# Kernel optimization log

Measured on AMD Instinct MI355X. Metric: run time of the kernel, lower is better.

Reference implementation:

```python
import jax, jax.numpy as jnp
import numpy as np
from jax import lax

RADIUS = 0.3
NSAMPLE = 16
NPOINT = 1024
NH = 1   # num_heading_bin
NS = 18  # num_size_cluster
EPS = 1e-5  # torch BatchNorm eps


def _bn(x, g, b, m, v):
    # eval-mode batchnorm over the last (channel) axis
    return (x - m) * (g / jnp.sqrt(v + EPS)) + b


def _fps(xyz, npoint):
    # furthest point sampling; xyz: (B,K,3) -> (B,npoint) int32 indices
    B, K, _ = xyz.shape
    def body(carry, _):
        dists, far = carry
        cur = jnp.take_along_axis(xyz, far[:, None, None], axis=1)  # (B,1,3)
        d = jnp.sum((xyz - cur) ** 2, -1)                           # (B,K)
        dists = jnp.minimum(dists, d)
        nxt = jnp.argmax(dists, -1).astype(jnp.int32)
        return (dists, nxt), far
    init = (jnp.full((B, K), 1e10, xyz.dtype), jnp.zeros((B,), jnp.int32))
    _, inds = lax.scan(body, init, None, length=npoint)
    return jnp.swapaxes(inds, 0, 1)  # (B, npoint)


def _ball_query(xyz, new_xyz):
    # first-NSAMPLE points within RADIUS of each center, pad with first hit
    K = xyz.shape[1]
    d2 = jnp.sum((new_xyz[:, :, None, :] - xyz[:, None, :, :]) ** 2, -1)  # (B,S,K)
    mask = d2 < RADIUS ** 2
    idx = jnp.where(mask, jnp.arange(K, dtype=jnp.int32)[None, None, :], K)
    idx = jnp.sort(idx, -1)[..., :NSAMPLE]
    first = idx[..., :1]
    idx = jnp.where(idx == K, first, idx)
    idx = jnp.where(idx == K, 0, idx)  # degenerate: no neighbor at all
    return idx  # (B,S,NSAMPLE)


def setup_inputs() -> dict:
    key = jax.random.key(0)
    ks = jax.random.split(key, 32)
    inp = {}
    inp['xyz'] = jax.random.normal(ks[0], (8, 8192, 3), jnp.float32)
    inp['features'] = jax.random.normal(ks[1], (8, 256, 8192), jnp.float32)
    i = 2
    # shared MLP: 259 -> 128 -> 128 -> 128 (conv2d 1x1, no bias, then BN)
    for l, (o, c) in enumerate([(128, 259), (128, 128), (128, 128)]):
        inp[f'mlp_w{l}'] = jax.random.normal(ks[i], (o, c), jnp.float32) * 0.1; i += 1
        inp[f'mlp_g{l}'] = jnp.ones((o,), jnp.float32)
        inp[f'mlp_b{l}'] = jnp.zeros((o,), jnp.float32)
        inp[f'mlp_m{l}'] = jax.random.normal(ks[i], (o,), jnp.float32) * 0.01; i += 1
        inp[f'mlp_v{l}'] = jax.random.uniform(ks[i], (o,), jnp.float32, 0.5, 1.5); i += 1
    # box head convs (conv1d k=1)
    for nm, (o, c) in [('c1', (128, 128)), ('c2', (128, 128)), ('c3', (97, 128))]:
        inp[f'{nm}_w'] = jax.random.normal(ks[i], (o, c), jnp.float32) * 0.1; i += 1
        inp[f'{nm}_b'] = jnp.zeros((o,), jnp.float32)
    for nm in ['bn1', 'bn2']:
        inp[f'{nm}_g'] = jnp.ones((128,), jnp.float32)
        inp[f'{nm}_b'] = jnp.zeros((128,), jnp.float32)
        inp[f'{nm}_m'] = jax.random.normal(ks[i], (128,), jnp.float32) * 0.01; i += 1
        inp[f'{nm}_v'] = jax.random.uniform(ks[i], (128,), jnp.float32, 0.5, 1.5); i += 1
    inp['mean_size_arr'] = jax.random.uniform(ks[i], (NS, 3), jnp.float32, 0.3, 2.0)
    return inp


def reference(xyz, features,
              mlp_w0, mlp_g0, mlp_b0, mlp_m0, mlp_v0,
              mlp_w1, mlp_g1, mlp_b1, mlp_m1, mlp_v1,
              mlp_w2, mlp_g2, mlp_b2, mlp_m2, mlp_v2,
              c1_w, c1_b, bn1_g, bn1_b, bn1_m, bn1_v,
              c2_w, c2_b, bn2_g, bn2_b, bn2_m, bn2_v,
              c3_w, c3_b, mean_size_arr):
    B = xyz.shape[0]
    # --- vote aggregation: FPS + ball query + group + shared MLP + maxpool ---
    fps_inds = _fps(xyz, NPOINT)
    new_xyz = jnp.take_along_axis(xyz, fps_inds[..., None], axis=1)  # (B,S,3)
    idx = _ball_query(xyz, new_xyz)                                  # (B,S,n)
    gather = jax.vmap(lambda a, i: a[i])
    g_xyz = (gather(xyz, idx) - new_xyz[:, :, None, :]) / RADIUS     # normalize_xyz
    g_f = gather(jnp.swapaxes(features, 1, 2), idx)                  # (B,S,n,256)
    h = jnp.concatenate([g_xyz, g_f], -1)                            # (B,S,n,259)
    for w, g, b, m, v in ((mlp_w0, mlp_g0, mlp_b0, mlp_m0, mlp_v0),
                          (mlp_w1, mlp_g1, mlp_b1, mlp_m1, mlp_v1),
                          (mlp_w2, mlp_g2, mlp_b2, mlp_m2, mlp_v2)):
        h = jax.nn.relu(_bn(jnp.einsum('bsnc,oc->bsno', h, w), g, b, m, v))
    feat = jnp.max(h, axis=2)                                        # (B,S,128)
    # --- box head (conv1d k=1 == per-point linear) ---
    net = jax.nn.relu(_bn(jnp.einsum('bsc,oc->bso', feat, c1_w) + c1_b,
                          bn1_g, bn1_b, bn1_m, bn1_v))
    net = jax.nn.relu(_bn(jnp.einsum('bsc,oc->bso', net, c2_w) + c2_b,
                          bn2_g, bn2_b, bn2_m, bn2_v))
    net = jnp.einsum('bsc,oc->bso', net, c3_w) + c3_b                # (B,S,97)
    # --- decode_scores ---
    obj = net[..., 0:2]
    center = new_xyz + net[..., 2:5]
    hs = net[..., 5:5 + NH]
    hr = net[..., 5 + NH:5 + 2 * NH] * (np.pi / NH)
    ss = net[..., 5 + 2 * NH:5 + 2 * NH + NS]
    srn = net[..., 5 + 2 * NH + NS:5 + 2 * NH + 4 * NS].reshape(B, NPOINT, NS, 3)
    sr = (srn * mean_size_arr[None, None]).reshape(B, NPOINT, NS * 3)
    sem = net[..., 5 + 2 * NH + 4 * NS:]
    return jnp.concatenate([obj, center, hs, hr, ss, sr, sem], -1)   # (B,S,97)
```

## Files before the change

### kernel.cpp

```cpp
#include <hip/hip_runtime.h>
#include <cstdint>
#include <cstddef>

#define BATCH   8
#define KPTS    8192
#define NPT     1024
#define NSAMP   16
#define RAD2    0.09f
#define HB      136
#define NWORK   248

typedef float f32x2 __attribute__((ext_vector_type(2)));
typedef float f32x4 __attribute__((ext_vector_type(4)));
typedef short s16x4 __attribute__((ext_vector_type(4)));
typedef short s16x8 __attribute__((ext_vector_type(8)));

__device__ __forceinline__ unsigned short f2bf(float x) {
    unsigned u = __float_as_uint(x);
    return (unsigned short)((u + 0x7fffu + ((u >> 16) & 1u)) >> 16);
}

template <int CTRL>
__device__ __forceinline__ float dppmaxf(float v) {
    int o = __builtin_amdgcn_update_dpp(0, __float_as_int(v), CTRL, 0xf, 0xf, true);
    return fmaxf(v, __int_as_float(o));
}

__device__ __forceinline__ int aload(int* p) {
    return __hip_atomic_load(p, __ATOMIC_ACQUIRE, __HIP_MEMORY_SCOPE_AGENT);
}
__device__ __forceinline__ void abump(int* p, int v) {
    __hip_atomic_fetch_add(p, v, __ATOMIC_RELEASE, __HIP_MEMORY_SCOPE_AGENT);
}

union __align__(16) SM {
    struct {
        float xs[KPTS], ys[KPTS], zs[KPTS];
        unsigned long long slot3[3];
        int hist[NPT];
    } fps;
    struct {
        float As[16 * 64];
        float Bs[16 * 130];
    } gemm;
    struct {
        unsigned short W1[128 * HB];
        unsigned short W2[128 * HB];
        unsigned short hbf[64 * HB];
        float gx[64], gy[64], gz[64];
        int   pidx[64];
        float s0[128], t0[128], wxs[128], wys[128], wzs[128];
        float s1[128], t1[128], s2[128], t2[128];
    } mlp;
};

__global__ __launch_bounds__(256, 1) void mega_kernel(
    const float* __restrict__ xyz, float* __restrict__ new_xyz,
    const float* __restrict__ feats, const float* __restrict__ w0,
    float* __restrict__ f0out,
    const float* __restrict__ g0, const float* __restrict__ b0,
    const float* __restrict__ m0, const float* __restrict__ v0,
    const float* __restrict__ w1,
    const float* __restrict__ g1, const float* __restrict__ b1a,
    const float* __restrict__ m1, const float* __restrict__ v1,
    const float* __restrict__ w2,
    const float* __restrict__ g2, const float* __restrict__ b2a,
    const float* __restrict__ m2, const float* __restrict__ v2,
    float* __restrict__ featout, int* __restrict__ cnt) {
    __shared__ SM sm;
    const int tid = threadIdx.x;
    const int bid = blockIdx.x;

    if (bid < 8) {
#pragma clang fp contract(off)
        const int b = bid;
        const float* xb = xyz + (size_t)b * KPTS * 3;

        for (int i = tid; i < KPTS; i += 256) {
            sm.fps.xs[i] = xb[i * 3 + 0];
            sm.fps.ys[i] = xb[i * 3 + 1];
            sm.fps.zs[i] = xb[i * 3 + 2];
        }
        if (tid < 3) sm.fps.slot3[tid] = 0ull;
        __syncthreads();

        const int base = tid << 5;
        f32x2 px[16], py[16], pz[16], dmn[16];
#pragma unroll
        for (int j = 0; j < 16; ++j) {
            int i0 = base + (j << 1);
            px[j] = (f32x2){sm.fps.xs[i0], sm.fps.xs[i0 + 1]};
            py[j] = (f32x2){sm.fps.ys[i0], sm.fps.ys[i0 + 1]};
            pz[j] = (f32x2){sm.fps.zs[i0], sm.fps.zs[i0 + 1]};
            dmn[j] = (f32x2){1e10f, 1e10f};
        }

        const int lane = tid & 63;
        int far = 0;
        int cur = 0, nxt = 1;
        for (int it = 0; it < NPT; ++it) {
            if (tid == 0) { sm.fps.hist[it] = far; sm.fps.slot3[nxt] = 0ull; }
            const float cx = sm.fps.xs[far], cy = sm.fps.ys[far], cz = sm.fps.zs[far];
            const f32x2 cx2 = (f32x2){cx, cx};
            const f32x2 cy2 = (f32x2){cy, cy};
            const f32x2 cz2 = (f32x2){cz, cz};

            f32x2 mm = (f32x2){-1.0f, -1.0f};
#pragma unroll
            for (int j = 0; j < 16; ++j) {
                f32x2 dx = px[j] - cx2;
                f32x2 dy = py[j] - cy2;
                f32x2 dz = pz[j] - cz2;
                f32x2 d  = (dx * dx + dy * dy) + dz * dz;
                f32x2 nd = __builtin_elementwise_min(dmn[j], d);
                dmn[j] = nd;
                mm = __builtin_elementwise_max(mm, nd);
            }
            float lmax = fmaxf(mm.x, mm.y);

            int ci = 0x7fffffff;
#pragma unroll
            for (int j = 0; j < 16; ++j) {
                if (dmn[j].x == lmax) ci = min(ci, base + (j << 1));
                if (dmn[j].y == lmax) ci = min(ci, base + (j << 1) + 1);
            }

            float wm = lmax;
            wm = dppmaxf<0x111>(wm);
            wm = dppmaxf<0x112>(wm);
            wm = dppmaxf<0x114>(wm);
            wm = dppmaxf<0x118>(wm);
            wm = dppmaxf<0x142>(wm);
            wm = dppmaxf<0x143>(wm);
            float wmax = __int_as_float(
                __builtin_amdgcn_readlane(__float_as_int(wm), 63));

            unsigned long long mk = __ballot(lmax == wmax);
            int wl = (int)__builtin_ctzll(mk);
            int cw = __builtin_amdgcn_readlane(ci, wl);

            if (lane == 0) {
                unsigned long long pk =
                    ((unsigned long long)__float_as_uint(wmax) << 32)
                    | (unsigned)(8191 - cw);
                atomicMax(&sm.fps.slot3[cur], pk);
            }
            __syncthreads();

            unsigned long long g = sm.fps.slot3[cur];
            far = 8191 - (int)(unsigned)(g & 0xffffffffull);
            cur = nxt;
            nxt = (nxt == 2) ? 0 : nxt + 1;

            if ((it & 31) == 31) {
                if (tid < 128) {
                    int c = tid & 3;
                    if (c < 3) {
                        int i = (it - 31) + (tid >> 2);
                        int idx = sm.fps.hist[i];
                        float v = (c == 0) ? sm.fps.xs[idx]
                                 : (c == 1) ? sm.fps.ys[idx] : sm.fps.zs[idx];
                        new_xyz[((size_t)b * NPT + i) * 3 + c] = v;
                    }
                }
                __threadfence();
                __syncthreads();
                if (tid == 0) abump(&cnt[b], 32);
            }
        }
        return;
    }

    const int wk = bid - 8;

    {
        const int rb = (tid >> 4) << 2;
        const int ob = tid & 15;
        for (int t = wk; t < 1024; t += NWORK) {
            const int b  = t >> 7;
            const int p0 = (t & 127) << 6;
            const float* fb = feats + (size_t)b * 256 * KPTS;

            float acc[4][8];
#pragma unroll
            for (int r = 0; r < 4; ++r)
#pragma unroll
                for (int c = 0; c < 8; ++c) acc[r][c] = 0.f;

            for (int k0 = 0; k0 < 256; k0 += 16) {
#pragma unroll
                for (int i = 0; i < 4; ++i) {
                    int e = tid + (i << 8);
                    int kk = e >> 6, pc = e & 63;
                    sm.gemm.As[kk * 64 + pc] = fb[(size_t)(k0 + kk) * KPTS + p0 + pc];
                }
#pragma unroll
                for (int i = 0; i < 8; ++i) {
                    int e = tid + (i << 8);
                    int o = e >> 4, kk = e & 15;
                    sm.gemm.Bs[kk * 130 + o] = w0[o * 259 + 3 + k0 + kk];
                }
                __syncthreads();
#pragma unroll
                for (int kk = 0; kk < 16; ++kk) {
                    float a[4], wvv[8];
#pragma unroll
                    for (int r = 0; r < 4; ++r) a[r] = sm.gemm.As[kk * 64 + rb + r];
#pragma unroll
                    for (int c = 0; c < 8; ++c) wvv[c] = sm.gemm.Bs[kk * 130 + ob + (c << 4)];
#pragma unroll
                    for (int r = 0; r < 4; ++r)
#pragma unroll
                        for (int c = 0; c < 8; ++c) acc[r][c] = fmaf(a[r], wvv[c], acc[r][c]);
                }
                __syncthreads();
            }
#pragma unroll
            for (int r = 0; r < 4; ++r) {
                float* outp = f0out + ((size_t)b * KPTS + p0 + rb + r) * 128 + ob;
#pragma unroll
                for (int c = 0; c < 8; ++c) outp[c << 4] = acc[r][c];
            }
        }
        __threadfence();
        __syncthreads();
        if (tid == 0) abump(&cnt[8], 1);
    }

    if (tid < 128) {
        float sc = g0[tid] / sqrtf(v0[tid] + 1e-5f);
        sm.mlp.s0[tid] = sc; sm.mlp.t0[tid] = b0[tid] - m0[tid] * sc;
        sc = g1[tid] / sqrtf(v1[tid] + 1e-5f);
        sm.mlp.s1[tid] = sc; sm.mlp.t1[tid] = b1a[tid] - m1[tid] * sc;
        sc = g2[tid] / sqrtf(v2[tid] + 1e-5f);
        sm.mlp.s2[tid] = sc; sm.mlp.t2[tid] = b2a[tid] - m2[tid] * sc;
        sm.mlp.wxs[tid] = w0[tid * 259 + 0];
        sm.mlp.wys[tid] = w0[tid * 259 + 1];
        sm.mlp.wzs[tid] = w0[tid * 259 + 2];
    }
#pragma unroll 4
    for (int i = 0; i < 16; ++i) {
        int e = tid + (i << 8);
        int o = e >> 5;
        int kt = (e & 31) << 2;
        float4 a4 = *(const float4*)(w1 + o * 128 + kt);
        s16x4 c4 = { (short)f2bf(a4.x), (short)f2bf(a4.y),
                     (short)f2bf(a4.z), (short)f2bf(a4.w) };
        *(s16x4*)&sm.mlp.W1[o * HB + kt] = c4;
        float4 b4 = *(const float4*)(w2 + o * 128 + kt);
        s16x4 d4 = { (short)f2bf(b4.x), (short)f2bf(b4.y),
                     (short)f2bf(b4.z), (short)f2bf(b4.w) };
        *(s16x4*)&sm.mlp.W2[o * HB + kt] = d4;
    }
    __syncthreads();

    const int lane = tid & 63;
    const int w    = tid >> 6;
    const int l15  = lane & 15;
    const int quad = lane >> 4;
    const int wrow = w << 4;

    for (int g = wk; g < 2048; g += NWORK) {
        const int b  = g & 7;
        const int qg = g >> 3;
        const int q0 = (b << 10) + (qg << 2);

        if (tid == 0) {
            while (aload(&cnt[8]) < NWORK) __builtin_amdgcn_s_sleep(16);
            const int need = (qg << 2) + 4;
            while (aload(&cnt[b]) < need) __builtin_amdgcn_s_sleep(16);
        }
        __syncthreads();

        {
            const int q = q0 + w;
            const float* xb = xyz + (size_t)b * KPTS * 3;
            const float qx = new_xyz[q * 3 + 0];
            const float qy = new_xyz[q * 3 + 1];
            const float qz = new_xyz[q * 3 + 2];
            int* op = &sm.mlp.pidx[w << 4];

            int total = 0;
            int first_p = 0;
            for (int c = 0; c < KPTS / 64; ++c) {
                int p = (c << 6) + lane;
                float pxv = xb[p * 3 + 0], pyv = xb[p * 3 + 1], pzv = xb[p * 3 + 2];
                float dx = __fsub_rn(qx, pxv), dy = __fsub_rn(qy, pyv), dz = __fsub_rn(qz, pzv);
                float d2 = __fadd_rn(__fadd_rn(__fmul_rn(dx, dx), __fmul_rn(dy, dy)),
                                     __fmul_rn(dz, dz));
                bool pred = d2 < RAD2;
                unsigned long long mask = __ballot(pred);
                if (total == 0 && mask != 0ull) first_p = (c << 6) + (int)__builtin_ctzll(mask);
                if (pred) {
                    int rank = (int)__popcll(mask & ((1ull << lane) - 1ull));
                    int slot = total + rank;
                    if (slot < NSAMP) op[slot] = p;
                }
                total += (int)__popcll(mask);
                if (total >= NSAMP) break;
            }
            if (total < NSAMP && lane >= total && lane < NSAMP) op[lane] = first_p;
        }
        __syncthreads();

        if (tid < 64) {
            int p = sm.mlp.pidx[tid];
            int q = q0 + (tid >> 4);
            const float* pp = xyz + ((size_t)b * KPTS + p) * 3;
            const float* nq = new_xyz + (size_t)q * 3;
            sm.mlp.gx[tid] = (pp[0] - nq[0]) / 0.3f;
            sm.mlp.gy[tid] = (pp[1] - nq[1]) / 0.3f;
            sm.mlp.gz[tid] = (pp[2] - nq[2]) / 0.3f;
        }
        __syncthreads();

#pragma unroll 2
        for (int i = 0; i < 8; ++i) {
            int e = tid + (i << 8);
            int row = e >> 5, o = (e & 31) << 2;
            int p = sm.mlp.pidx[row];
            float4 v4 = *(const float4*)(f0out + ((size_t)b * KPTS + p) * 128 + o);
            float gxr = sm.mlp.gx[row], gyr = sm.mlp.gy[row], gzr = sm.mlp.gz[row];
            float r0 = fmaf(sm.mlp.wzs[o + 0], gzr, fmaf(sm.mlp.wys[o + 0], gyr, fmaf(sm.mlp.wxs[o + 0], gxr, v4.x)));
            float r1 = fmaf(sm.mlp.wzs[o + 1], gzr, fmaf(sm.mlp.wys[o + 1], gyr, fmaf(sm.mlp.wxs[o + 1], gxr, v4.y)));
            float r2 = fmaf(sm.mlp.wzs[o + 2], gzr, fmaf(sm.mlp.wys[o + 2], gyr, fmaf(sm.mlp.wxs[o + 2], gxr, v4.z)));
            float r3 = fmaf(sm.mlp.wzs[o + 3], gzr, fmaf(sm.mlp.wys[o + 3], gyr, fmaf(sm.mlp.wxs[o + 3], gxr, v4.w)));
            s16x4 c4;
            c4.x = (short)f2bf(fmaxf(fmaf(r0, sm.mlp.s0[o + 0], sm.mlp.t0[o + 0]), 0.f));
            c4.y = (short)f2bf(fmaxf(fmaf(r1, sm.mlp.s0[o + 1], sm.mlp.t0[o + 1]), 0.f));
            c4.z = (short)f2bf(fmaxf(fmaf(r2, sm.mlp.s0[o + 2], sm.mlp.t0[o + 2]), 0.f));
            c4.w = (short)f2bf(fmaxf(fmaf(r3, sm.mlp.s0[o + 3], sm.mlp.t0[o + 3]), 0.f));
            *(s16x4*)&sm.mlp.hbf[row * HB + o] = c4;
        }
        __syncthreads();

        f32x4 acc[8];
#pragma unroll
        for (int t = 0; t < 8; ++t) acc[t] = (f32x4){0.f, 0.f, 0.f, 0.f};
#pragma unroll
        for (int k0 = 0; k0 < 128; k0 += 32) {
            s16x8 a = *(const s16x8*)&sm.mlp.hbf[(wrow + l15) * HB + k0 + (quad << 3)];
#pragma unroll
            for (int t = 0; t < 8; ++t) {
                s16x8 bf = *(const s16x8*)&sm.mlp.W1[((t << 4) + l15) * HB + k0 + (quad << 3)];
                acc[t] = __builtin_amdgcn_mfma_f32_16x16x32_bf16(a, bf, acc[t], 0, 0, 0);
            }
        }
        __syncthreads();

#pragma unroll
        for (int t = 0; t < 8; ++t) {
            int o = (t << 4) + l15;
            float ss = sm.mlp.s1[o], tt = sm.mlp.t1[o];
#pragma unroll
            for (int r = 0; r < 4; ++r) {
                float v = fmaxf(fmaf(acc[t][r], ss, tt), 0.f);
                sm.mlp.hbf[(wrow + (quad << 2) + r) * HB + o] = f2bf(v);
            }
        }
        __syncthreads();

#pragma unroll
        for (int t = 0; t < 8; ++t) acc[t] = (f32x4){0.f, 0.f, 0.f, 0.f};
#pragma unroll
        for (int k0 = 0; k0 < 128; k0 += 32) {
            s16x8 a = *(const s16x8*)&sm.mlp.hbf[(wrow + l15) * HB + k0 + (quad << 3)];
#pragma unroll
            for (int t = 0; t < 8; ++t) {
                s16x8 bf = *(const s16x8*)&sm.mlp.W2[((t << 4) + l15) * HB + k0 + (quad << 3)];
                acc[t] = __builtin_amdgcn_mfma_f32_16x16x32_bf16(a, bf, acc[t], 0, 0, 0);
            }
        }

#pragma unroll
        for (int t = 0; t < 8; ++t) {
            int o = (t << 4) + l15;
            float ss = sm.mlp.s2[o], tt = sm.mlp.t2[o];
            float m0v = fmaxf(fmaf(acc[t][0], ss, tt), 0.f);
            float m1v = fmaxf(fmaf(acc[t][1], ss, tt), 0.f);
            float m2v = fmaxf(fmaf(acc[t][2], ss, tt), 0.f);
            float m3v = fmaxf(fmaf(acc[t][3], ss, tt), 0.f);
            float m = fmaxf(fmaxf(m0v, m1v), fmaxf(m2v, m3v));
            m = fmaxf(m, __shfl_xor(m, 16));
            m = fmaxf(m, __shfl_xor(m, 32));
            if (quad == 0)
                featout[(size_t)(q0 + w) * 128 + o] = m;
        }
    }
}

__global__ __launch_bounds__(256) void head_kernel(
    const float* __restrict__ feat, const float* __restrict__ new_xyz,
    const float* __restrict__ c1w, const float* __restrict__ c1b,
    const float* __restrict__ c2w, const float* __restrict__ c2b,
    const float* __restrict__ c3w, const float* __restrict__ c3b,
    const float* __restrict__ bg1, const float* __restrict__ bb1,
    const float* __restrict__ bm1, const float* __restrict__ bv1,
    const float* __restrict__ bg2, const float* __restrict__ bb2,
    const float* __restrict__ bm2, const float* __restrict__ bv2,
    const float* __restrict__ msz, float* __restrict__ out) {
    const int tid = threadIdx.x;
    const int q0  = blockIdx.x << 3;
    __shared__ float fs[8][128], n1[8][128], n2[8][128];
    __shared__ float s1[128], t1[128], s2[128], t2[128], ms[54];

#pragma unroll
    for (int i = 0; i < 4; ++i) {
        int e = tid + (i << 8);
        fs[e >> 7][e & 127] = feat[(size_t)q0 * 128 + e];
    }
    if (tid < 128) {
        float sc = bg1[tid] / sqrtf(bv1[tid] + 1e-5f);
        s1[tid] = sc; t1[tid] = bb1[tid] - bm1[tid] * sc;
        sc = bg2[tid] / sqrtf(bv2[tid] + 1e-5f);
        s2[tid] = sc; t2[tid] = bb2[tid] - bm2[tid] * sc;
    }
    if (tid < 54) ms[tid] = msz[tid];
    __syncthreads();

    const int o    = tid & 127;
    const int half = tid >> 7;

    {
        float a[4];
#pragma unroll
        for (int j = 0; j < 4; ++j) a[j] = c1b[o];
        const float* wr = c1w + o * 128;
        for (int k = 0; k < 128; k += 4) {
            float4 w4 = *(const float4*)(wr + k);
#pragma unroll
            for (int j = 0; j < 4; ++j) {
                int qq = half * 4 + j;
                a[j] = fmaf(fs[qq][k + 0], w4.x, a[j]);
                a[j] = fmaf(fs[qq][k + 1], w4.y, a[j]);
                a[j] = fmaf(fs[qq][k + 2], w4.z, a[j]);
                a[j] = fmaf(fs[qq][k + 3], w4.w, a[j]);
            }
        }
#pragma unroll
        for (int j = 0; j < 4; ++j)
            n1[half * 4 + j][o] = fmaxf(fmaf(a[j], s1[o], t1[o]), 0.f);
    }
    __syncthreads();
    {
        float a[4];
#pragma unroll
        for (int j = 0; j < 4; ++j) a[j] = c2b[o];
        const float* wr = c2w + o * 128;
        for (int k = 0; k < 128; k += 4) {
            float4 w4 = *(const float4*)(wr + k);
#pragma unroll
            for (int j = 0; j < 4; ++j) {
                int qq = half * 4 + j;
                a[j] = fmaf(n1[qq][k + 0], w4.x, a[j]);
                a[j] = fmaf(n1[qq][k + 1], w4.y, a[j]);
                a[j] = fmaf(n1[qq][k + 2], w4.z, a[j]);
                a[j] = fmaf(n1[qq][k + 3], w4.w, a[j]);
            }
        }
#pragma unroll
        for (int j = 0; j < 4; ++j)
            n2[half * 4 + j][o] = fmaxf(fmaf(a[j], s2[o], t2[o]), 0.f);
    }
    __syncthreads();
    if (o < 97) {
        float a[4];
#pragma unroll
        for (int j = 0; j < 4; ++j) a[j] = c3b[o];
        const float* wr = c3w + o * 128;
        for (int k = 0; k < 128; k += 4) {
            float4 w4 = *(const float4*)(wr + k);
#pragma unroll
            for (int j = 0; j < 4; ++j) {
                int qq = half * 4 + j;
                a[j] = fmaf(n2[qq][k + 0], w4.x, a[j]);
                a[j] = fmaf(n2[qq][k + 1], w4.y, a[j]);
                a[j] = fmaf(n2[qq][k + 2], w4.z, a[j]);
                a[j] = fmaf(n2[qq][k + 3], w4.w, a[j]);
            }
        }
#pragma unroll
        for (int j = 0; j < 4; ++j) {
            int q = q0 + half * 4 + j;
            float v = a[j];
            if (o >= 2 && o < 5) v += new_xyz[(size_t)q * 3 + (o - 2)];
            else if (o == 6) v *= 3.14159265358979323846f;
            else if (o >= 25 && o < 79) v *= ms[o - 25];
            out[(size_t)q * 97 + o] = v;
        }
    }
}

extern "C" void kernel_launch(void* const* d_in, const int* in_sizes, int n_in,
                              void* d_out, int out_size, void* d_ws, size_t ws_size,
                              hipStream_t stream) {
    const float* xyz      = (const float*)d_in[0];
    const float* features = (const float*)d_in[1];
    const float* w0  = (const float*)d_in[2];
    const float* g0  = (const float*)d_in[3];
    const float* b0  = (const float*)d_in[4];
    const float* m0  = (const float*)d_in[5];
    const float* v0  = (const float*)d_in[6];
    const float* w1  = (const float*)d_in[7];
    const float* g1  = (const float*)d_in[8];
    const float* b1  = (const float*)d_in[9];
    const float* m1  = (const float*)d_in[10];
    const float* v1  = (const float*)d_in[11];
    const float* w2  = (const float*)d_in[12];
    const float* g2  = (const float*)d_in[13];
    const float* b2  = (const float*)d_in[14];
    const float* m2  = (const float*)d_in[15];
    const float* v2  = (const float*)d_in[16];
    const float* c1w = (const float*)d_in[17];
    const float* c1b = (const float*)d_in[18];
    const float* c2w = (const float*)d_in[19];
    const float* c2b = (const float*)d_in[20];
    const float* c3w = (const float*)d_in[21];
    const float* c3b = (const float*)d_in[22];
    const float* bg1 = (const float*)d_in[23];
    const float* bb1 = (const float*)d_in[24];
    const float* bm1 = (const float*)d_in[25];
    const float* bv1 = (const float*)d_in[26];
    const float* bg2 = (const float*)d_in[27];
    const float* bb2 = (const float*)d_in[28];
    const float* bm2 = (const float*)d_in[29];
    const float* bv2 = (const float*)d_in[30];
    const float* msz = (const float*)d_in[31];

    float* F0   = (float*)d_ws;
    float* feat = F0 + (size_t)BATCH * KPTS * 128;
    int*   cnt  = (int*)(feat + (size_t)BATCH * NPT * 128);
    float* nxyz = (float*)(cnt + (size_t)BATCH * NPT * NSAMP);
    float* outp = (float*)d_out;

    hipMemsetAsync(cnt, 0, 16 * sizeof(int), stream);
    mega_kernel<<<256, 256, 0, stream>>>(
        xyz, nxyz, features, w0, F0,
        g0, b0, m0, v0, w1, g1, b1, m1, v1, w2, g2, b2, m2, v2,
        feat, cnt);
    head_kernel <<<BATCH * NPT / 8, 256, 0, stream>>>(
        feat, nxyz, c1w, c1b, c2w, c2b, c3w, c3b,
        bg1, bb1, bm1, bv1, bg2, bb2, bm2, bv2, msz, outp);
}
```

Before: 1.259 ms.

## Fuse box-head MLP into mega kernel per 4-center tile

Removes the separate head_kernel launch and the global round-trip of the pooled 128-dim features. Each mega_kernel work tile now keeps its 4 max-pooled feature rows in shared memory and runs the three box-head linear layers, BN, ReLU and the decode step in place. This trades a kernel launch and feature traffic for extra barriers and serial head work inside the persistent loop. The head's weights are also re-read per 4-center tile instead of per 8, and the head now runs on only 248 blocks rather than 1024.

```diff
diff --git a/kernel.cpp b/kernel.cpp
--- a/kernel.cpp
+++ b/kernel.cpp
@@ -51,6 +51,9 @@
         int   pidx[64];
         float s0[128], t0[128], wxs[128], wys[128], wzs[128];
         float s1[128], t1[128], s2[128], t2[128];
+        float s3[128], t3[128], s4[128], t4[128];
+        float fs[4][128], n1[4][128], n2[4][128];
+        float ms[54];
     } mlp;
 };
 
@@ -66,7 +69,15 @@
     const float* __restrict__ w2,
     const float* __restrict__ g2, const float* __restrict__ b2a,
     const float* __restrict__ m2, const float* __restrict__ v2,
-    float* __restrict__ featout, int* __restrict__ cnt) {
+    const float* __restrict__ c1w, const float* __restrict__ c1b,
+    const float* __restrict__ c2w, const float* __restrict__ c2b,
+    const float* __restrict__ c3w, const float* __restrict__ c3b,
+    const float* __restrict__ bg1, const float* __restrict__ bb1,
+    const float* __restrict__ bm1, const float* __restrict__ bv1,
+    const float* __restrict__ bg2, const float* __restrict__ bb2,
+    const float* __restrict__ bm2, const float* __restrict__ bv2,
+    const float* __restrict__ msz, float* __restrict__ out,
+    int* __restrict__ cnt) {
     __shared__ SM sm;
     const int tid = threadIdx.x;
     const int bid = blockIdx.x;
@@ -234,10 +245,15 @@
         sm.mlp.s1[tid] = sc; sm.mlp.t1[tid] = b1a[tid] - m1[tid] * sc;
         sc = g2[tid] / sqrtf(v2[tid] + 1e-5f);
         sm.mlp.s2[tid] = sc; sm.mlp.t2[tid] = b2a[tid] - m2[tid] * sc;
+        sc = bg1[tid] / sqrtf(bv1[tid] + 1e-5f);
+        sm.mlp.s3[tid] = sc; sm.mlp.t3[tid] = bb1[tid] - bm1[tid] * sc;
+        sc = bg2[tid] / sqrtf(bv2[tid] + 1e-5f);
+        sm.mlp.s4[tid] = sc; sm.mlp.t4[tid] = bb2[tid] - bm2[tid] * sc;
         sm.mlp.wxs[tid] = w0[tid * 259 + 0];
         sm.mlp.wys[tid] = w0[tid * 259 + 1];
         sm.mlp.wzs[tid] = w0[tid * 259 + 2];
     }
+    if (tid < 54) sm.mlp.ms[tid] = msz[tid];
 #pragma unroll 4
     for (int i = 0; i < 16; ++i) {
         int e = tid + (i << 8);
@@ -383,111 +399,81 @@
             float m = fmaxf(fmaxf(m0v, m1v), fmaxf(m2v, m3v));
             m = fmaxf(m, __shfl_xor(m, 16));
             m = fmaxf(m, __shfl_xor(m, 32));
-            if (quad == 0)
-                featout[(size_t)(q0 + w) * 128 + o] = m;
-        }
-    }
-}
-
-__global__ __launch_bounds__(256) void head_kernel(
-    const float* __restrict__ feat, const float* __restrict__ new_xyz,
-    const float* __restrict__ c1w, const float* __restrict__ c1b,
-    const float* __restrict__ c2w, const float* __restrict__ c2b,
-    const float* __restrict__ c3w, const float* __restrict__ c3b,
-    const float* __restrict__ bg1, const float* __restrict__ bb1,
-    const float* __restrict__ bm1, const float* __restrict__ bv1,
-    const float* __restrict__ bg2, const float* __restrict__ bb2,
-    const float* __restrict__ bm2, const float* __restrict__ bv2,
-    const float* __restrict__ msz, float* __restrict__ out) {
-    const int tid = threadIdx.x;
-    const int q0  = blockIdx.x << 3;
-    __shared__ float fs[8][128], n1[8][128], n2[8][128];
-    __shared__ float s1[128], t1[128], s2[128], t2[128], ms[54];
-
-#pragma unroll
-    for (int i = 0; i < 4; ++i) {
-        int e = tid + (i << 8);
-        fs[e >> 7][e & 127] = feat[(size_t)q0 * 128 + e];
-    }
-    if (tid < 128) {
-        float sc = bg1[tid] / sqrtf(bv1[tid] + 1e-5f);
-        s1[tid] = sc; t1[tid] = bb1[tid] - bm1[tid] * sc;
-        sc = bg2[tid] / sqrtf(bv2[tid] + 1e-5f);
-        s2[tid] = sc; t2[tid] = bb2[tid] - bm2[tid] * sc;
-    }
-    if (tid < 54) ms[tid] = msz[tid];
-    __syncthreads();
-
-    const int o    = tid & 127;
-    const int half = tid >> 7;
-
-    {
-        float a[4];
-#pragma unroll
-        for (int j = 0; j < 4; ++j) a[j] = c1b[o];
-        const float* wr = c1w + o * 128;
-        for (int k = 0; k < 128; k += 4) {
-            float4 w4 = *(const float4*)(wr + k);
-#pragma unroll
-            for (int j = 0; j < 4; ++j) {
-                int qq = half * 4 + j;
-                a[j] = fmaf(fs[qq][k + 0], w4.x, a[j]);
-                a[j] = fmaf(fs[qq][k + 1], w4.y, a[j]);
-                a[j] = fmaf(fs[qq][k + 2], w4.z, a[j]);
-                a[j] = fmaf(fs[qq][k + 3], w4.w, a[j]);
-            }
-        }
-#pragma unroll
-        for (int j = 0; j < 4; ++j)
-            n1[half * 4 + j][o] = fmaxf(fmaf(a[j], s1[o], t1[o]), 0.f);
-    }
-    __syncthreads();
-    {
-        float a[4];
-#pragma unroll
-        for (int j = 0; j < 4; ++j) a[j] = c2b[o];
-        const float* wr = c2w + o * 128;
-        for (int k = 0; k < 128; k += 4) {
-            float4 w4 = *(const float4*)(wr + k);
-#pragma unroll
-            for (int j = 0; j < 4; ++j) {
-                int qq = half * 4 + j;
-                a[j] = fmaf(n1[qq][k + 0], w4.x, a[j]);
-                a[j] = fmaf(n1[qq][k + 1], w4.y, a[j]);
-                a[j] = fmaf(n1[qq][k + 2], w4.z, a[j]);
-                a[j] = fmaf(n1[qq][k + 3], w4.w, a[j]);
-            }
-        }
-#pragma unroll
-        for (int j = 0; j < 4; ++j)
-            n2[half * 4 + j][o] = fmaxf(fmaf(a[j], s2[o], t2[o]), 0.f);
-    }
-    __syncthreads();
-    if (o < 97) {
-        float a[4];
-#pragma unroll
-        for (int j = 0; j < 4; ++j) a[j] = c3b[o];
-        const float* wr = c3w + o * 128;
-        for (int k = 0; k < 128; k += 4) {
-            float4 w4 = *(const float4*)(wr + k);
-#pragma unroll
-            for (int j = 0; j < 4; ++j) {
-                int qq = half * 4 + j;
-                a[j] = fmaf(n2[qq][k + 0], w4.x, a[j]);
-                a[j] = fmaf(n2[qq][k + 1], w4.y, a[j]);
-                a[j] = fmaf(n2[qq][k + 2], w4.z, a[j]);
-                a[j] = fmaf(n2[qq][k + 3], w4.w, a[j]);
-            }
-        }
-#pragma unroll
-        for (int j = 0; j < 4; ++j) {
-            int q = q0 + half * 4 + j;
-            float v = a[j];
-            if (o >= 2 && o < 5) v += new_xyz[(size_t)q * 3 + (o - 2)];
-            else if (o == 6) v *= 3.14159265358979323846f;
-            else if (o >= 25 && o < 79) v *= ms[o - 25];
-            out[(size_t)q * 97 + o] = v;
-        }
+            if (quad == 0) sm.mlp.fs[w][o] = m;
+        }
+        __syncthreads();
+
+        const int o    = tid & 127;
+        const int half = tid >> 7;
+        {
+            float a[2];
+#pragma unroll
+            for (int j = 0; j < 2; ++j) a[j] = c1b[o];
+            const float* wr = c1w + o * 128;
+            for (int k = 0; k < 128; k += 4) {
+                float4 w4 = *(const float4*)(wr + k);
+#pragma unroll
+                for (int j = 0; j < 2; ++j) {
+                    int qq = half * 2 + j;
+                    a[j] = fmaf(sm.mlp.fs[qq][k + 0], w4.x, a[j]);
+                    a[j] = fmaf(sm.mlp.fs[qq][k + 1], w4.y, a[j]);
+                    a[j] = fmaf(sm.mlp.fs[qq][k + 2], w4.z, a[j]);
+                    a[j] = fmaf(sm.mlp.fs[qq][k + 3], w4.w, a[j]);
+                }
+            }
+#pragma unroll
+            for (int j = 0; j < 2; ++j)
+                sm.mlp.n1[half * 2 + j][o] = fmaxf(fmaf(a[j], sm.mlp.s3[o], sm.mlp.t3[o]), 0.f);
+        }
+        __syncthreads();
+        {
+            float a[2];
+#pragma unroll
+            for (int j = 0; j < 2; ++j) a[j] = c2b[o];
+            const float* wr = c2w + o * 128;
+            for (int k = 0; k < 128; k += 4) {
+                float4 w4 = *(const float4*)(wr + k);
+#pragma unroll
+                for (int j = 0; j < 2; ++j) {
+                    int qq = half * 2 + j;
+                    a[j] = fmaf(sm.mlp.n1[qq][k + 0], w4.x, a[j]);
+                    a[j] = fmaf(sm.mlp.n1[qq][k + 1], w4.y, a[j]);
+                    a[j] = fmaf(sm.mlp.n1[qq][k + 2], w4.z, a[j]);
+                    a[j] = fmaf(sm.mlp.n1[qq][k + 3], w4.w, a[j]);
+                }
+            }
+#pragma unroll
+            for (int j = 0; j < 2; ++j)
+                sm.mlp.n2[half * 2 + j][o] = fmaxf(fmaf(a[j], sm.mlp.s4[o], sm.mlp.t4[o]), 0.f);
+        }
+        __syncthreads();
+        if (o < 97) {
+            float a[2];
+#pragma unroll
+            for (int j = 0; j < 2; ++j) a[j] = c3b[o];
+            const float* wr = c3w + o * 128;
+            for (int k = 0; k < 128; k += 4) {
+                float4 w4 = *(const float4*)(wr + k);
+#pragma unroll
+                for (int j = 0; j < 2; ++j) {
+                    int qq = half * 2 + j;
+                    a[j] = fmaf(sm.mlp.n2[qq][k + 0], w4.x, a[j]);
+                    a[j] = fmaf(sm.mlp.n2[qq][k + 1], w4.y, a[j]);
+                    a[j] = fmaf(sm.mlp.n2[qq][k + 2], w4.z, a[j]);
+                    a[j] = fmaf(sm.mlp.n2[qq][k + 3], w4.w, a[j]);
+                }
+            }
+#pragma unroll
+            for (int j = 0; j < 2; ++j) {
+                int q = q0 + half * 2 + j;
+                float v = a[j];
+                if (o >= 2 && o < 5) v += new_xyz[(size_t)q * 3 + (o - 2)];
+                else if (o == 6) v *= 3.14159265358979323846f;
+                else if (o >= 25 && o < 79) v *= sm.mlp.ms[o - 25];
+                out[(size_t)q * 97 + o] = v;
+            }
+        }
+        __syncthreads();
     }
 }
 
@@ -537,8 +523,7 @@
     mega_kernel<<<256, 256, 0, stream>>>(
         xyz, nxyz, features, w0, F0,
         g0, b0, m0, v0, w1, g1, b1, m1, v1, w2, g2, b2, m2, v2,
-        feat, cnt);
-    head_kernel <<<BATCH * NPT / 8, 256, 0, stream>>>(
-        feat, nxyz, c1w, c1b, c2w, c2b, c3w, c3b,
-        bg1, bb1, bm1, bv1, bg2, bb2, bm2, bv2, msz, outp);
+        c1w, c1b, c2w, c2b, c3w, c3b,
+        bg1, bb1, bm1, bv1, bg2, bb2, bm2, bv2, msz, outp,
+        cnt);
 }
```

Result: faster. 1.203 ms (median of 2 runs) (-4.4%).
